# Optimization experiments

Hardware: AMD Instinct MI355X
Metric: run time of the kernel (lower is better)

Reference implementation:

```python
import jax, jax.numpy as jnp
import numpy as np

H0, W0 = 256, 256
B = 8
N_EV = 100000
N_PARAMS = 4000000
SMOOTHNESS_WEIGHT = 0.5
WEIGHT_DECAY_WEIGHT = 1e-4


def setup_inputs() -> dict:
    key = jax.random.key(0)
    ks = jax.random.split(key, 11)
    d = {}
    for i in range(4):
        s = 2 ** (3 - i)
        d['flow%d' % i] = jax.random.normal(ks[i], (B, 2, H0 // s, W0 // s), jnp.float32)
    d['xs'] = jax.random.randint(ks[4], (B, N_EV), 0, W0).astype(jnp.int32)
    d['ys'] = jax.random.randint(ks[5], (B, N_EV), 0, H0).astype(jnp.int32)
    # timestamps sorted ascending so t[-1]/t[0] are the last/first event times
    d['ts'] = jnp.sort(jax.random.uniform(ks[6], (B, N_EV), jnp.float32), axis=1)
    # polarity in {-1, +1}
    d['ps'] = (2 * jax.random.randint(ks[7], (B, N_EV), 0, 2) - 1).astype(jnp.int32)
    d['frame'] = jax.random.normal(ks[8], (B, 1, H0, W0), jnp.float32)
    d['frame_'] = jax.random.normal(ks[9], (B, 1, H0, W0), jnp.float32)
    d['params'] = jax.random.normal(ks[10], (N_PARAMS,), jnp.float32) * 0.01
    return d


def _event_loss(x, y, t, mask, flow, forward):
    # x, y: int32 [N] in-range coords for this flow scale; t: float [N];
    # mask: bool [N] selecting the polarity subset; flow: [2, H, W].
    # Masked events contribute zero weight instead of being sliced out
    # (shape-stable equivalent of torch boolean indexing).
    eps = jnp.finfo(flow.dtype).eps
    H, W = flow.shape[1], flow.shape[2]
    n = t.shape[0]
    mf = mask.astype(flow.dtype)
    if forward:
        t_ref = t[n - 1 - jnp.argmax(mask[::-1])]  # t[-1] of masked subset
        t_ = t_ref - t + eps
    else:
        t_ref = t[jnp.argmax(mask)]  # t[0] of masked subset
        t_ = t_ref - t - eps
    fx = flow[0, y, x]
    fy = flow[1, y, x]
    x_ = jnp.clip(x.astype(flow.dtype) + t_ * fx, 0.0, W - 1.0)
    y_ = jnp.clip(y.astype(flow.dtype) + t_ * fy, 0.0, H - 1.0)
    x0 = jnp.floor(x_); x1 = x0 + 1.0
    y0 = jnp.floor(y_); y1 = y0 + 1.0
    x0w = x_ - x0; x1w = x1 - x_
    y0w = y_ - y0; y1w = y1 - y_
    tm = t * mf
    Ta = x0w * y0w * tm
    Tb = x1w * y0w * tm
    Tc = x0w * y1w * tm
    Td = x1w * y1w * tm
    x1i = jnp.minimum(x1, W - 1.0).astype(jnp.int32)
    y1i = jnp.minimum(y1, H - 1.0).astype(jnp.int32)
    x0i = x0.astype(jnp.int32); y0i = y0.astype(jnp.int32)
    Ia = x1i + y1i * W
    Ib = x0i + y1i * W
    Ic = x1i + y0i * W
    Id = x0i + y0i * W
    idxs = jnp.concatenate([Ia, Ib, Ic, Id])
    vals = jnp.concatenate([Ta, Tb, Tc, Td])
    den = jnp.zeros(H * W, flow.dtype).at[idxs].add(jnp.tile(mf, 4))
    num = jnp.zeros(H * W, flow.dtype).at[idxs].add(vals)
    r = num / (den + eps)
    return jnp.sum(jnp.sqrt(r * r + 1e-06))


def _compute_event_flow_loss(xs, ys, ts, ps, flows):
    total = jnp.float32(0.0)
    pos = ps == 1
    neg = ps == -1
    for fi, flow in enumerate(flows):  # 4 scales, structurally distinct shapes
        scale = 2 ** (3 - fi)
        x = (xs.astype(jnp.float32) / scale).astype(jnp.int32)
        y = (ys.astype(jnp.float32) / scale).astype(jnp.int32)
        for mask in (pos, neg):
            for fwd in (True, False):
                f = lambda xb, yb, tb, mb, fb, fwd=fwd: _event_loss(xb, yb, tb, mb, fb, fwd)
                total = total + jnp.sum(jax.vmap(f)(x, y, ts, mask, flow))
    return total


def _charbonnier(d):
    # alpha=0.45, epsilon=1e-3 -> epsilon**2 = 1e-6
    return jnp.mean((d * d + 1e-06) ** 0.45)


def _smoothness(flow):
    lr = _charbonnier(flow[..., :, 1:] - flow[..., :, :-1])
    ud = _charbonnier(flow[..., 1:, :] - flow[..., :-1, :])
    d1 = _charbonnier(flow[..., 1:, 1:] - flow[..., :-1, :-1])
    d2 = _charbonnier(flow[..., :-1, 1:] - flow[..., 1:, :-1])
    return (lr + ud + d1 + d2) / 4.0


def reference(flow0, flow1, flow2, flow3, xs, ys, ts, ps, frame, frame_, params):
    flows = [flow0, flow1, flow2, flow3]
    weight_decay_loss = jnp.sum(params ** 2) / 2.0 * WEIGHT_DECAY_WEIGHT
    smoothness_loss = sum(_smoothness(f) for f in flows) * (SMOOTHNESS_WEIGHT / 4.0)
    event_loss = _compute_event_flow_loss(xs, ys, ts, ps, flows)
    return weight_decay_loss + event_loss + smoothness_loss * 200.0
```

## Files before the change

### kernel.cpp

```cpp
#include <hip/hip_runtime.h>
#include <math.h>
#include <limits.h>

#define NEV 100000
#define NB 8
#define NSL 32
#define SLEV (NEV / NSL)
#define F32EPS 1.1920929e-7f
#define SCALE 524288.0f
#define INV_SCALE (1.0f/524288.0f)

typedef unsigned long long u64;

#define OFF_BINSTART 6400000
#define OFF_TREF     6401056
#define OFF_FI0P     6401184
#define OFF_FI1P     7449760
#define OFF_HISTG    11644064
#define OFF_MMG      11775136
#define OFF_MISCP    11779232

#define MISC_BLOCKS 1024

__device__ __forceinline__ void lds_add64(u64* p, u64 v) {
    __hip_atomic_fetch_add(p, v, __ATOMIC_RELAXED, __HIP_MEMORY_SCOPE_WORKGROUP);
}
__device__ __forceinline__ int lds_add32(int* p, int v) {
    return __hip_atomic_fetch_add(p, v, __ATOMIC_RELAXED, __HIP_MEMORY_SCOPE_WORKGROUP);
}

__device__ __forceinline__ float pow045(float z) {
    return __builtin_amdgcn_exp2f(0.45f * __builtin_amdgcn_logf(z));
}

__global__ __launch_bounds__(256) void k_front(
    const int* __restrict__ ys, const int* __restrict__ ps,
    const float* __restrict__ params, int nP,
    const float* __restrict__ f0, const float* __restrict__ f1,
    const float* __restrict__ f2, const float* __restrict__ f3,
    int* __restrict__ histG, int* __restrict__ mmG, float* __restrict__ miscP) {
    int tid = threadIdx.x;
    int bid = blockIdx.x;
    __shared__ int hist[4][32];
    __shared__ int mm[4];
    __shared__ float red[4];

    if (bid < 256) {
        int b = bid & 7;
        int sl = bid >> 3;
        int w = tid >> 6, lane = tid & 63;
        const int* yb = ys + b * NEV + sl * SLEV;
        const int* pb = ps + b * NEV + sl * SLEV;

        if (tid < 128) hist[tid >> 5][tid & 31] = 0;
        if (tid == 0) { mm[0] = INT_MAX; mm[1] = -1; mm[2] = INT_MAX; mm[3] = -1; }
        __syncthreads();

        int mnP = INT_MAX, mxP = -1, mnN = INT_MAX, mxN = -1;
        int gbase = sl * SLEV;
        for (int i = w * 64 + lane; i < SLEV; i += 256) {
            int p = pb[i];
            int y = yb[i];
            int m = (p == 1) ? 0 : 1;
            lds_add32(&hist[w][m * 16 + (y >> 4)], 1);
            int gi = gbase + i;
            if (m == 0) { mnP = min(mnP, gi); mxP = max(mxP, gi); }
            else        { mnN = min(mnN, gi); mxN = max(mxN, gi); }
        }
        for (int o = 32; o > 0; o >>= 1) {
            mnP = min(mnP, __shfl_down(mnP, o, 64));
            mxP = max(mxP, __shfl_down(mxP, o, 64));
            mnN = min(mnN, __shfl_down(mnN, o, 64));
            mxN = max(mxN, __shfl_down(mxN, o, 64));
        }
        if (lane == 0) {
            atomicMin(&mm[0], mnP); atomicMax(&mm[1], mxP);
            atomicMin(&mm[2], mnN); atomicMax(&mm[3], mxN);
        }
        __syncthreads();
        if (tid < 128) histG[(bid * 4 + (tid >> 5)) * 32 + (tid & 31)] = hist[tid >> 5][tid & 31];
        if (tid < 4)   mmG[bid * 4 + tid] = mm[tid];
        return;
    }

    float s = 0.0f;
    int gtid = (bid - 256) * 256 + tid;
    const int gstride = MISC_BLOCKS * 256;

    int n4 = nP >> 2;
    const float4* p4 = (const float4*)params;
    float wsum = 0.0f;
    for (int i = gtid; i < n4; i += gstride) {
        float4 v = p4[i];
        wsum += v.x * v.x + v.y * v.y + v.z * v.z + v.w * v.w;
    }
    if (gtid == 0) for (int i = n4 * 4; i < nP; ++i) wsum += params[i] * params[i];
    s += wsum * 5e-5f;

    const int nTot = 1392640;
    for (int idx = gtid; idx < nTot; idx += gstride) {
        int fi, off, logW;
        if (idx < 16384)       { fi = 0; off = 0;      logW = 5; }
        else if (idx < 81920)  { fi = 1; off = 16384;  logW = 6; }
        else if (idx < 344064) { fi = 2; off = 81920;  logW = 7; }
        else                   { fi = 3; off = 344064; logW = 8; }
        const float* f = (fi == 0) ? f0 : (fi == 1) ? f1 : (fi == 2) ? f2 : f3;
        int W = 1 << logW;
        int local = idx - off;
        int x = local & (W - 1);
        int y = (local >> logW) & (W - 1);
        float c_lr = 6.25f / (float)(16 * W * (W - 1));
        float c_dd = 6.25f / (float)(16 * (W - 1) * (W - 1));
        float v = f[local];
        bool xok = x < W - 1;
        bool yok = y < W - 1;
        float vr = xok ? f[local + 1] : 0.0f;
        float vd = yok ? f[local + W] : 0.0f;
        if (xok) { float d = vr - v; s += c_lr * pow045(d * d + 1e-6f); }
        if (yok) { float d = vd - v; s += c_lr * pow045(d * d + 1e-6f); }
        if (xok && yok) {
            float d1 = f[local + W + 1] - v;
            s += c_dd * pow045(d1 * d1 + 1e-6f);
            float d2 = vr - vd;
            s += c_dd * pow045(d2 * d2 + 1e-6f);
        }
    }

    for (int o = 32; o > 0; o >>= 1) s += __shfl_down(s, o, 64);
    if ((tid & 63) == 0) red[tid >> 6] = s;
    __syncthreads();
    if (tid == 0) miscP[bid - 256] = red[0] + red[1] + red[2] + red[3];
}

__global__ __launch_bounds__(256) void k_scatter(
    const int* __restrict__ xs, const int* __restrict__ ys,
    const float* __restrict__ ts, const int* __restrict__ ps,
    const int* __restrict__ histG, const int* __restrict__ mmG,
    uint2* __restrict__ bins, int* __restrict__ binStart,
    float* __restrict__ tref, float* __restrict__ out) {
    int bid = blockIdx.x;
    int tid = threadIdx.x;
    __shared__ int hh[4096];
    __shared__ int curs[4][32];
    __shared__ int binTot[32];
    __shared__ int binBase[32];
    __shared__ int mm[4];

    int b = (bid < 256) ? (bid & 7) : (bid - 256);

    for (int i = tid; i < 4096; i += 256)
        hh[i] = histG[(i >> 7) * 1024 + b * 128 + (i & 127)];
    __syncthreads();

    if (bid >= 256) {
        if (tid < 32) {
            int tot = 0;
            for (int sl2 = 0; sl2 < 32; ++sl2) {
                #pragma unroll
                for (int w2 = 0; w2 < 4; ++w2) tot += hh[sl2 * 128 + w2 * 32 + tid];
            }
            binTot[tid] = tot;
        }
        __syncthreads();
        if (tid == 0) {
            int run = 0;
            for (int k = 0; k < 32; ++k) { binStart[b * 33 + k] = run; run += binTot[k]; }
            binStart[b * 33 + 32] = run;
            if (bid == 256) out[0] = 0.0f;
        }
        if (tid >= 64 && tid < 68) {
            int c = tid - 64;
            int v = (c == 0 || c == 2) ? INT_MAX : -1;
            for (int sl2 = 0; sl2 < 32; ++sl2) {
                int x = mmG[(sl2 * 8 + b) * 4 + c];
                v = (c == 0 || c == 2) ? min(v, x) : max(v, x);
            }
            mm[c] = v;
        }
        __syncthreads();
        if (tid == 64) {
            const float* tb = ts + b * NEV;
            int mnP = mm[0], mxP = mm[1], mnN = mm[2], mxN = mm[3];
            int fP = (mnP == INT_MAX) ? 0 : mnP;
            int lP = (mxP < 0) ? (NEV - 1) : mxP;
            int fN = (mnN == INT_MAX) ? 0 : mnN;
            int lN = (mxN < 0) ? (NEV - 1) : mxN;
            tref[b * 4 + 0] = tb[lP];
            tref[b * 4 + 1] = tb[fP];
            tref[b * 4 + 2] = tb[lN];
            tref[b * 4 + 3] = tb[fN];
        }
        return;
    }

    int sl = bid >> 3;
    if (tid < 128) {
        int w = tid >> 5, bin = tid & 31;
        int pre = 0, tot = 0, wpre = 0;
        for (int sl2 = 0; sl2 < 32; ++sl2) {
            #pragma unroll
            for (int w2 = 0; w2 < 4; ++w2) {
                int v = hh[sl2 * 128 + w2 * 32 + bin];
                tot += v;
                if (sl2 < sl) pre += v;
                if (sl2 == sl && w2 < w) wpre += v;
            }
        }
        if (w == 0) binTot[bin] = tot;
        curs[w][bin] = pre + wpre;
    }
    __syncthreads();
    if (tid == 0) {
        int run = 0;
        for (int k = 0; k < 32; ++k) { binBase[k] = run; run += binTot[k]; }
    }
    __syncthreads();
    if (tid < 128) curs[tid >> 5][tid & 31] += binBase[tid & 31];
    __syncthreads();

    const int*   xb = xs + b * NEV + sl * SLEV;
    const int*   yb = ys + b * NEV + sl * SLEV;
    const float* tb = ts + b * NEV + sl * SLEV;
    const int*   pb = ps + b * NEV + sl * SLEV;
    uint2* ob = bins + b * NEV;
    int w = tid >> 6, lane = tid & 63;

    for (int i = w * 64 + lane; i < SLEV; i += 256) {
        int p = pb[i];
        int x = xb[i];
        int y = yb[i];
        float t = tb[i];
        int m = (p == 1) ? 0 : 1;
        int bin = m * 16 + (y >> 4);
        int pos = lds_add32(&curs[w][bin], 1);
        ob[pos] = make_uint2((unsigned)(x | (y << 8)), __float_as_uint(t));
    }
}

__global__ __launch_bounds__(1024) void k_splat(
    const float* __restrict__ f0, const float* __restrict__ f1,
    const float* __restrict__ f2, const float* __restrict__ f3,
    const uint2* __restrict__ bins, const int* __restrict__ binStart,
    const float* __restrict__ tref,
    u64* __restrict__ fi0P, u64* __restrict__ fi1P,
    float* __restrict__ out) {
    __shared__ u64 acc[8192];
    __shared__ float red[16];

    int tid = threadIdx.x;
    int bid = blockIdx.x;
    int b = bid & 7;
    int rm = bid >> 3;
    int m = rm & 1;
    int role = rm >> 1;
    int bm = b * 2 + m;

    int fi, row0 = 0, nrows, lo, hi, slice = 0, nslice = 1, mode;
    if (role < 4)       { fi = 0; mode = 0; slice = role;     nslice = 4; nrows = 32; lo = 0; hi = 15; }
    else if (role < 8)  { fi = 1; mode = 0; slice = role - 4; nslice = 4; nrows = 64; lo = 0; hi = 15; }
    else if (role < 16) { int c = role - 8;  fi = 2; mode = 1; row0 = 16 * c; nrows = 16;
                          lo = max(0, 2 * c - 1); hi = min(15, 2 * c + 2); }
    else                { int c = role - 16; fi = 3; mode = 1; row0 = 16 * c; nrows = 16;
                          lo = max(0, c - 1); hi = min(15, c + 1); }

    int W = 32 << fi;
    int sh = 3 - fi;
    int planeN = (fi == 0) ? 1024 : (fi == 1) ? 4096 : nrows * W;
    int used = (fi == 0) ? 8192 : 2 * planeN;
    int rowEnd = row0 + nrows;
    float Wm1 = (float)(W - 1);

    const float* flow = (fi == 0) ? f0 : (fi == 1) ? f1 : (fi == 2) ? f2 : f3;
    const float* fxp = flow + (size_t)b * 2 * W * W;
    const float* fyp = fxp + W * W;

    for (int i = tid; i < used; i += 1024) acc[i] = 0ULL;
    __syncthreads();

    float trF = tref[b * 4 + m * 2 + 0];
    float trB = tref[b * 4 + m * 2 + 1];

    int s0 = binStart[b * 33 + m * 16 + lo];
    int e0 = binStart[b * 33 + m * 16 + hi + 1];
    const uint2* eb = bins + b * NEV;

    int rep = (fi == 0) ? (((tid >> 4) & 3) * 2048) : 0;

    for (int i = s0 + slice * 1024 + tid; i < e0; i += nslice * 1024) {
        uint2 ev = eb[i];
        int x = ev.x & 255;
        int y = (ev.x >> 8) & 255;
        float t = __uint_as_float(ev.y);
        int xi = x >> sh, yi = y >> sh;
        float fx = fxp[yi * W + xi];
        float fy = fyp[yi * W + xi];
        float tF = trF - t + F32EPS;
        float tB = trB - t - F32EPS;
        #pragma unroll
        for (int dir = 0; dir < 2; ++dir) {
            float t_ = dir ? tB : tF;
            float x_ = fminf(fmaxf((float)xi + t_ * fx, 0.0f), Wm1);
            float y_ = fminf(fmaxf((float)yi + t_ * fy, 0.0f), Wm1);
            float x0f = floorf(x_), y0f = floorf(y_);
            float x0w = x_ - x0f, x1w = 1.0f - x0w;
            float y0w = y_ - y0f, y1w = 1.0f - y0w;
            int x0i = (int)x0f, y0i = (int)y0f;
            int x1i = min(x0i + 1, W - 1);
            int y1i = min(y0i + 1, W - 1);
            u64 Pa = (1ULL << 32) | (u64)(unsigned)(x0w * y0w * t * SCALE);
            u64 Pb = (1ULL << 32) | (u64)(unsigned)(x1w * y0w * t * SCALE);
            u64 Pc = (1ULL << 32) | (u64)(unsigned)(x0w * y1w * t * SCALE);
            u64 Pd = (1ULL << 32) | (u64)(unsigned)(x1w * y1w * t * SCALE);
            int base = rep + dir * planeN;
            if (mode == 0) {
                int r1 = base + y1i * W;
                int r0 = base + y0i * W;
                lds_add64(&acc[r1 + x1i], Pa);
                lds_add64(&acc[r1 + x0i], Pb);
                lds_add64(&acc[r0 + x1i], Pc);
                lds_add64(&acc[r0 + x0i], Pd);
            } else {
                if (y1i >= row0 && y1i < rowEnd) {
                    int r = base + (y1i - row0) * W;
                    lds_add64(&acc[r + x1i], Pa);
                    lds_add64(&acc[r + x0i], Pb);
                }
                if (y0i >= row0 && y0i < rowEnd) {
                    int r = base + (y0i - row0) * W;
                    lds_add64(&acc[r + x1i], Pc);
                    lds_add64(&acc[r + x0i], Pd);
                }
            }
        }
    }
    __syncthreads();

    if (mode == 0) {
        if (fi == 0) {
            for (int j = tid; j < 2048; j += 1024)
                fi0P[(bm * 4 + slice) * 2048 + j] =
                    acc[j] + acc[j + 2048] + acc[j + 4096] + acc[j + 6144];
        } else {
            for (int j = tid; j < 8192; j += 1024)
                fi1P[(bm * 4 + slice) * 8192 + j] = acc[j];
        }
        return;
    }

    float s = 0.0f;
    for (int j = tid; j < used; j += 1024) {
        u64 v = acc[j];
        float num = (float)(unsigned)(v & 0xffffffffULL) * INV_SCALE;
        float den = (float)(unsigned)(v >> 32);
        float r = num / (den + F32EPS);
        s += sqrtf(r * r + 1e-6f);
    }
    for (int o = 32; o > 0; o >>= 1) s += __shfl_down(s, o, 64);
    if ((tid & 63) == 0) red[tid >> 6] = s;
    __syncthreads();
    if (tid == 0) {
        float tot = 0.0f;
        for (int w2 = 0; w2 < 16; ++w2) tot += red[w2];
        atomicAdd(out, tot);
    }
}

__global__ __launch_bounds__(256) void k_merge(const u64* __restrict__ fi0P,
                                               const u64* __restrict__ fi1P,
                                               const float* __restrict__ miscP,
                                               float* __restrict__ out) {
    int idx = blockIdx.x * 256 + threadIdx.x;
    u64 v = 0;
    if (idx < 32768) {
        int bm = idx >> 11, j = idx & 2047;
        const u64* p = fi0P + (bm * 4) * 2048 + j;
        #pragma unroll
        for (int s = 0; s < 4; ++s) v += p[s * 2048];
    } else {
        int r = idx - 32768;
        int bm = r >> 13, j = r & 8191;
        const u64* p = fi1P + (bm * 4) * 8192 + j;
        #pragma unroll
        for (int s = 0; s < 4; ++s) v += p[s * 8192];
    }
    float num = (float)(unsigned)(v & 0xffffffffULL) * INV_SCALE;
    float den = (float)(unsigned)(v >> 32);
    float r = num / (den + F32EPS);
    float s = sqrtf(r * r + 1e-6f);

    if (blockIdx.x == 0) {
        float ms = miscP[threadIdx.x] + miscP[threadIdx.x + 256]
                 + miscP[threadIdx.x + 512] + miscP[threadIdx.x + 768];
        s += ms;
    }

    for (int o = 32; o > 0; o >>= 1) s += __shfl_down(s, o, 64);
    __shared__ float red[4];
    if ((threadIdx.x & 63) == 0) red[threadIdx.x >> 6] = s;
    __syncthreads();
    if (threadIdx.x == 0)
        atomicAdd(out, red[0] + red[1] + red[2] + red[3]);
}

extern "C" void kernel_launch(void* const* d_in, const int* in_sizes, int n_in,
                              void* d_out, int out_size, void* d_ws, size_t ws_size,
                              hipStream_t stream) {
    const float* f0 = (const float*)d_in[0];
    const float* f1 = (const float*)d_in[1];
    const float* f2 = (const float*)d_in[2];
    const float* f3 = (const float*)d_in[3];
    const int*   xs = (const int*)d_in[4];
    const int*   ys = (const int*)d_in[5];
    const float* ts = (const float*)d_in[6];
    const int*   ps = (const int*)d_in[7];
    const float* params = (const float*)d_in[10];
    float* out = (float*)d_out;

    char* ws = (char*)d_ws;
    uint2* bins     = (uint2*)ws;
    int*   binStart = (int*)(ws + OFF_BINSTART);
    float* tref     = (float*)(ws + OFF_TREF);
    u64*   fi0P     = (u64*)(ws + OFF_FI0P);
    u64*   fi1P     = (u64*)(ws + OFF_FI1P);
    int*   histG    = (int*)(ws + OFF_HISTG);
    int*   mmG      = (int*)(ws + OFF_MMG);
    float* miscP    = (float*)(ws + OFF_MISCP);

    hipLaunchKernelGGL(k_front, dim3(256 + MISC_BLOCKS), dim3(256), 0, stream,
                       ys, ps, params, in_sizes[10], f0, f1, f2, f3, histG, mmG, miscP);
    hipLaunchKernelGGL(k_scatter, dim3(264), dim3(256), 0, stream,
                       xs, ys, ts, ps, histG, mmG, bins, binStart, tref, out);
    hipLaunchKernelGGL(k_splat, dim3(512), dim3(1024), 0, stream,
                       f0, f1, f2, f3, bins, binStart, tref, fi0P, fi1P, out);
    hipLaunchKernelGGL(k_merge, dim3(640), dim3(256), 0, stream, fi0P, fi1P, miscP, out);
}
```

Measured before the change: 154.8 us.

## Fold merge kernel into splat via global atomics and last-block finalize

Drops the separate k_merge launch. The mode-0 splat blocks now atomically add their partial u64 accumulators into shared global planes, which k_front zeroes. The last block to finish, found through an atomic counter, then computes the final sqrt reduction and adds in the misc partials. k_front's smoothness loop also assigns fixed block ranges to each flow scale, so the per-element branch on scale goes away. This saves one launch and the partial-plane write and readback, but adds global 64-bit atomic contention. The whole 160K-element finalize now runs serially inside a single 1024-thread block, which could create a tail.

Result: slower. 209.5 us (+35.3%).

```diff
diff --git a/kernel.cpp b/kernel.cpp
--- a/kernel.cpp
+++ b/kernel.cpp
@@ -14,11 +14,12 @@
 
 #define OFF_BINSTART 6400000
 #define OFF_TREF     6401056
-#define OFF_FI0P     6401184
-#define OFF_FI1P     7449760
-#define OFF_HISTG    11644064
-#define OFF_MMG      11775136
-#define OFF_MISCP    11779232
+#define OFF_FI0S     6401184
+#define OFF_FI1S     6663328
+#define OFF_HISTG    7711904
+#define OFF_MMG      7842976
+#define OFF_MISCP    7847072
+#define OFF_CTR      7851168
 
 #define MISC_BLOCKS 1024
 
@@ -38,7 +39,8 @@
     const float* __restrict__ params, int nP,
     const float* __restrict__ f0, const float* __restrict__ f1,
     const float* __restrict__ f2, const float* __restrict__ f3,
-    int* __restrict__ histG, int* __restrict__ mmG, float* __restrict__ miscP) {
+    int* __restrict__ histG, int* __restrict__ mmG, float* __restrict__ miscP,
+    u64* __restrict__ fi0S, u64* __restrict__ fi1S, int* __restrict__ ctr) {
     int tid = threadIdx.x;
     int bid = blockIdx.x;
     __shared__ int hist[4][32];
@@ -83,34 +85,48 @@
         return;
     }
 
+    int bid2 = bid - 256;
+
+    {
+        int zi = bid2 * 256 + tid;
+        if (zi < 32768)  fi0S[zi] = 0ULL;
+        int z1 = zi;
+        if (z1 < 131072) fi1S[z1] = 0ULL;
+        if (zi == 0) *ctr = 0;
+    }
+
     float s = 0.0f;
-    int gtid = (bid - 256) * 256 + tid;
-    const int gstride = MISC_BLOCKS * 256;
-
-    int n4 = nP >> 2;
-    const float4* p4 = (const float4*)params;
-    float wsum = 0.0f;
-    for (int i = gtid; i < n4; i += gstride) {
-        float4 v = p4[i];
-        wsum += v.x * v.x + v.y * v.y + v.z * v.z + v.w * v.w;
-    }
-    if (gtid == 0) for (int i = n4 * 4; i < nP; ++i) wsum += params[i] * params[i];
-    s += wsum * 5e-5f;
-
-    const int nTot = 1392640;
-    for (int idx = gtid; idx < nTot; idx += gstride) {
-        int fi, off, logW;
-        if (idx < 16384)       { fi = 0; off = 0;      logW = 5; }
-        else if (idx < 81920)  { fi = 1; off = 16384;  logW = 6; }
-        else if (idx < 344064) { fi = 2; off = 81920;  logW = 7; }
-        else                   { fi = 3; off = 344064; logW = 8; }
-        const float* f = (fi == 0) ? f0 : (fi == 1) ? f1 : (fi == 2) ? f2 : f3;
-        int W = 1 << logW;
-        int local = idx - off;
+    {
+        int gtid = bid2 * 256 + tid;
+        const int gstride = MISC_BLOCKS * 256;
+        int n4 = nP >> 2;
+        const float4* p4 = (const float4*)params;
+        float wsum = 0.0f;
+        for (int i = gtid; i < n4; i += gstride) {
+            float4 v = p4[i];
+            wsum += v.x * v.x + v.y * v.y + v.z * v.z + v.w * v.w;
+        }
+        if (gtid == 0) for (int i = n4 * 4; i < nP; ++i) wsum += params[i] * params[i];
+        s += wsum * 5e-5f;
+    }
+
+    int fi, R, r0;
+    if (bid2 < 768)       { fi = 3; R = 768; r0 = 0; }
+    else if (bid2 < 960)  { fi = 2; R = 192; r0 = 768; }
+    else if (bid2 < 1008) { fi = 1; R = 48;  r0 = 960; }
+    else                  { fi = 0; R = 16;  r0 = 1008; }
+    const int logW = 5 + fi;
+    const int W = 1 << logW;
+    const int count = 16 << (2 * logW);
+    const float* f = (fi == 0) ? f0 : (fi == 1) ? f1 : (fi == 2) ? f2 : f3;
+    const float c_lr = 6.25f / (float)(16 * W * (W - 1));
+    const float c_dd = 6.25f / (float)(16 * (W - 1) * (W - 1));
+    const int g0 = (bid2 - r0) * 256 + tid;
+    const int gs = R * 256;
+
+    for (int local = g0; local < count; local += gs) {
         int x = local & (W - 1);
         int y = (local >> logW) & (W - 1);
-        float c_lr = 6.25f / (float)(16 * W * (W - 1));
-        float c_dd = 6.25f / (float)(16 * (W - 1) * (W - 1));
         float v = f[local];
         bool xok = x < W - 1;
         bool yok = y < W - 1;
@@ -129,7 +145,7 @@
     for (int o = 32; o > 0; o >>= 1) s += __shfl_down(s, o, 64);
     if ((tid & 63) == 0) red[tid >> 6] = s;
     __syncthreads();
-    if (tid == 0) miscP[bid - 256] = red[0] + red[1] + red[2] + red[3];
+    if (tid == 0) miscP[bid2] = red[0] + red[1] + red[2] + red[3];
 }
 
 __global__ __launch_bounds__(256) void k_scatter(
@@ -242,10 +258,12 @@
     const float* __restrict__ f2, const float* __restrict__ f3,
     const uint2* __restrict__ bins, const int* __restrict__ binStart,
     const float* __restrict__ tref,
-    u64* __restrict__ fi0P, u64* __restrict__ fi1P,
+    u64* __restrict__ fi0S, u64* __restrict__ fi1S,
+    const float* __restrict__ miscP, int* __restrict__ ctr,
     float* __restrict__ out) {
     __shared__ u64 acc[8192];
     __shared__ float red[16];
+    __shared__ int shT;
 
     int tid = threadIdx.x;
     int bid = blockIdx.x;
@@ -337,12 +355,42 @@
 
     if (mode == 0) {
         if (fi == 0) {
-            for (int j = tid; j < 2048; j += 1024)
-                fi0P[(bm * 4 + slice) * 2048 + j] =
-                    acc[j] + acc[j + 2048] + acc[j + 4096] + acc[j + 6144];
+            u64* plane = fi0S + bm * 2048;
+            for (int j = tid; j < 2048; j += 1024) {
+                u64 v = acc[j] + acc[j + 2048] + acc[j + 4096] + acc[j + 6144];
+                if (v) atomicAdd(&plane[j], v);
+            }
         } else {
-            for (int j = tid; j < 8192; j += 1024)
-                fi1P[(bm * 4 + slice) * 8192 + j] = acc[j];
+            u64* plane = fi1S + bm * 8192;
+            for (int j = tid; j < 8192; j += 1024) {
+                u64 v = acc[j];
+                if (v) atomicAdd(&plane[j], v);
+            }
+        }
+        __syncthreads();
+        if (tid == 0) {
+            __threadfence();
+            shT = atomicAdd(ctr, 1);
+        }
+        __syncthreads();
+        if (shT == 127) {
+            __threadfence();
+            float s = miscP[tid];
+            for (int idx = tid; idx < 163840; idx += 1024) {
+                u64 v = (idx < 32768) ? fi0S[idx] : fi1S[idx - 32768];
+                float num = (float)(unsigned)(v & 0xffffffffULL) * INV_SCALE;
+                float den = (float)(unsigned)(v >> 32);
+                float r = num / (den + F32EPS);
+                s += sqrtf(r * r + 1e-6f);
+            }
+            for (int o = 32; o > 0; o >>= 1) s += __shfl_down(s, o, 64);
+            if ((tid & 63) == 0) red[tid >> 6] = s;
+            __syncthreads();
+            if (tid == 0) {
+                float tot = 0.0f;
+                for (int w2 = 0; w2 < 16; ++w2) tot += red[w2];
+                atomicAdd(out, tot);
+            }
         }
         return;
     }
@@ -363,43 +411,6 @@
         for (int w2 = 0; w2 < 16; ++w2) tot += red[w2];
         atomicAdd(out, tot);
     }
-}
-
-__global__ __launch_bounds__(256) void k_merge(const u64* __restrict__ fi0P,
-                                               const u64* __restrict__ fi1P,
-                                               const float* __restrict__ miscP,
-                                               float* __restrict__ out) {
-    int idx = blockIdx.x * 256 + threadIdx.x;
-    u64 v = 0;
-    if (idx < 32768) {
-        int bm = idx >> 11, j = idx & 2047;
-        const u64* p = fi0P + (bm * 4) * 2048 + j;
-        #pragma unroll
-        for (int s = 0; s < 4; ++s) v += p[s * 2048];
-    } else {
-        int r = idx - 32768;
-        int bm = r >> 13, j = r & 8191;
-        const u64* p = fi1P + (bm * 4) * 8192 + j;
-        #pragma unroll
-        for (int s = 0; s < 4; ++s) v += p[s * 8192];
-    }
-    float num = (float)(unsigned)(v & 0xffffffffULL) * INV_SCALE;
-    float den = (float)(unsigned)(v >> 32);
-    float r = num / (den + F32EPS);
-    float s = sqrtf(r * r + 1e-6f);
-
-    if (blockIdx.x == 0) {
-        float ms = miscP[threadIdx.x] + miscP[threadIdx.x + 256]
-                 + miscP[threadIdx.x + 512] + miscP[threadIdx.x + 768];
-        s += ms;
-    }
-
-    for (int o = 32; o > 0; o >>= 1) s += __shfl_down(s, o, 64);
-    __shared__ float red[4];
-    if ((threadIdx.x & 63) == 0) red[threadIdx.x >> 6] = s;
-    __syncthreads();
-    if (threadIdx.x == 0)
-        atomicAdd(out, red[0] + red[1] + red[2] + red[3]);
 }
 
 extern "C" void kernel_launch(void* const* d_in, const int* in_sizes, int n_in,
@@ -420,17 +431,19 @@
     uint2* bins     = (uint2*)ws;
     int*   binStart = (int*)(ws + OFF_BINSTART);
     float* tref     = (float*)(ws + OFF_TREF);
-    u64*   fi0P     = (u64*)(ws + OFF_FI0P);
-    u64*   fi1P     = (u64*)(ws + OFF_FI1P);
+    u64*   fi0S     = (u64*)(ws + OFF_FI0S);
+    u64*   fi1S     = (u64*)(ws + OFF_FI1S);
     int*   histG    = (int*)(ws + OFF_HISTG);
     int*   mmG      = (int*)(ws + OFF_MMG);
     float* miscP    = (float*)(ws + OFF_MISCP);
+    int*   ctr      = (int*)(ws + OFF_CTR);
 
     hipLaunchKernelGGL(k_front, dim3(256 + MISC_BLOCKS), dim3(256), 0, stream,
-                       ys, ps, params, in_sizes[10], f0, f1, f2, f3, histG, mmG, miscP);
+                       ys, ps, params, in_sizes[10], f0, f1, f2, f3,
+                       histG, mmG, miscP, fi0S, fi1S, ctr);
     hipLaunchKernelGGL(k_scatter, dim3(264), dim3(256), 0, stream,
                        xs, ys, ts, ps, histG, mmG, bins, binStart, tref, out);
     hipLaunchKernelGGL(k_splat, dim3(512), dim3(1024), 0, stream,
-                       f0, f1, f2, f3, bins, binStart, tref, fi0P, fi1P, out);
-    hipLaunchKernelGGL(k_merge, dim3(640), dim3(256), 0, stream, fi0P, fi1P, miscP, out);
-}
+                       f0, f1, f2, f3, bins, binStart, tref,
+                       fi0S, fi1S, miscP, ctr, out);
+}
```
